# Kernel tuning notes

Hardware: AMD Instinct MI355X
Metric: run time of the kernel (lower is better)

Reference implementation:

```python
import jax, jax.numpy as jnp
import numpy as np
from jax import lax


def binarize_weight(w):
    # per-output-channel scaling alpha = mean(|w|), binary weight = sign(w)*alpha
    alpha = jnp.mean(jnp.abs(w), axis=(1, 2, 3), keepdims=True)  # [O,1,1,1]
    wb = jnp.sign(w) * alpha
    # STE: forward uses wb, gradient passes straight through to w
    return w + lax.stop_gradient(wb - w)


def pixel_unshuffle2(x):
    # NCHW, factor 2: out[:, c*4 + i*2 + j] = x[:, c, i::2, j::2]
    B, C, H, W = x.shape
    x = x.reshape(B, C, H // 2, 2, W // 2, 2)
    x = x.transpose(0, 1, 3, 5, 2, 4)
    return x.reshape(B, C * 4, H // 2, W // 2)


def setup_inputs() -> dict:
    key = jax.random.key(0)
    ks = jax.random.split(key, 5)
    x = jax.random.normal(ks[0], (16, 256, 128, 128), dtype=jnp.float32)
    conv_w = jax.random.normal(ks[1], (128, 256, 3, 3), dtype=jnp.float32) * 0.05
    move1_b = jax.random.normal(ks[2], (128,), dtype=jnp.float32) * 0.01
    prelu_w = jax.random.uniform(ks[3], (128,), dtype=jnp.float32) * 0.25
    move2_b = jax.random.normal(ks[4], (128,), dtype=jnp.float32) * 0.01
    scale = jnp.ones((1,), dtype=jnp.float32)
    return {"x": x, "conv_w": conv_w, "move1_b": move1_b,
            "prelu_w": prelu_w, "move2_b": move2_b, "scale": scale}


def reference(x, conv_w, move1_b, prelu_w, move2_b, scale):
    wb = binarize_weight(conv_w)
    out = lax.conv_general_dilated(
        x, wb, window_strides=(1, 1), padding=((1, 1), (1, 1)),
        dimension_numbers=("NCHW", "OIHW", "NCHW"))  # [B,128,H,W]
    out = out + move1_b[None, :, None, None]
    a = prelu_w[None, :, None, None]
    out = jnp.where(out > 0, out, a * out)
    out = out + move2_b[None, :, None, None]
    shortcut = x[:, : x.shape[1] // 2, :, :] * scale[0]
    out = out + shortcut
    return pixel_unshuffle2(out)  # [B,512,H/2,W/2]
```

## Files before the change

### kernel.cpp

```cpp
#include <hip/hip_runtime.h>
#include <stdint.h>

typedef unsigned short ushort_t;
typedef __bf16 bf16x8 __attribute__((ext_vector_type(8)));
typedef float f32x4 __attribute__((ext_vector_type(4)));

#define NB   16
#define CIN  256
#define COUT 128
#define HH   128
#define WW   128
#define HP   130
#define WP   130
#define KTAP 9
#define KTOT 2304

__device__ __forceinline__ ushort_t f2bf(float f) {
  union { float f; uint32_t u; } v; v.f = f;
  uint32_t u = v.u;
  uint32_t r = (u + 0x7fffu + ((u >> 16) & 1u)) >> 16;
  return (ushort_t)r;
}
__device__ __forceinline__ float bf2f(ushort_t b) {
  union { uint32_t u; float f; } v; v.u = ((uint32_t)b) << 16;
  return v.f;
}
__device__ __forceinline__ void gload_lds16(const void* g, void* l) {
  __builtin_amdgcn_global_load_lds((const __attribute__((address_space(1))) void*)g,
                                   (__attribute__((address_space(3))) void*)l, 16, 0, 0);
}

__global__ void prep_w_kernel(const float* __restrict__ w,
                              ushort_t* __restrict__ sgnW,
                              float* __restrict__ alpha) {
  int o = blockIdx.x, t = threadIdx.x;
  float s = 0.f;
  for (int e = t; e < KTOT; e += 256) {
    float v = w[o * KTOT + e];
    s += fabsf(v);
    ushort_t sg = (v > 0.f) ? 0x3F80 : (v < 0.f ? 0xBF80 : 0);
    int c = e / 9;
    int tap = e - c * 9;
    sgnW[(tap * COUT + o) * CIN + c] = sg;
  }
  __shared__ float red[4];
  for (int off = 32; off; off >>= 1) s += __shfl_down(s, off, 64);
  if ((t & 63) == 0) red[t >> 6] = s;
  __syncthreads();
  if (t == 0) alpha[o] = (red[0] + red[1] + red[2] + red[3]) / (float)KTOT;
}

__global__ void transpose_kernel(const float* __restrict__ x,
                                 ushort_t* __restrict__ xT) {
  int bid = blockIdx.x;
  int ct = bid & 3;
  int wt = (bid >> 2) & 1;
  int h  = (bid >> 3) & 127;
  int b  = bid >> 10;
  int c0 = ct * 64, w0 = wt * 64;
  __shared__ float tile[64][65];
  int t = threadIdx.x;
  int wl = t & 63, cl4 = t >> 6;
  const float* src = x + (((size_t)b * CIN + c0) * HH + h) * WW + w0;
  for (int it = 0; it < 16; ++it) {
    int cl = it * 4 + cl4;
    tile[cl][wl] = src[(size_t)cl * (HH * WW) + wl];
  }
  __syncthreads();
  int cp = t & 31, wi = t >> 5;
  for (int it = 0; it < 8; ++it) {
    int wl2 = it * 8 + wi;
    int cl = cp * 2;
    uint32_t pk = (uint32_t)f2bf(tile[cl][wl2]) |
                  ((uint32_t)f2bf(tile[cl + 1][wl2]) << 16);
    size_t idx = ((((size_t)b * HP + h + 1) * WP) + (w0 + wl2 + 1)) * CIN + c0 + cl;
    *(uint32_t*)(xT + idx) = pk;
  }
}

__global__ __launch_bounds__(256, 2) void conv_gemm(
    const ushort_t* __restrict__ xT, const ushort_t* __restrict__ sgnW,
    const float* __restrict__ alpha, const float* __restrict__ mv1,
    const float* __restrict__ pw, const float* __restrict__ mv2,
    const float* __restrict__ scale, float* __restrict__ out) {
  __shared__ __align__(16) ushort_t As[128 * 64];
  __shared__ __align__(16) ushort_t Bs[128 * 64];

  int bid = blockIdx.x;
  int wg = ((bid & 7) << 8) | (bid >> 3);
  int b = wg >> 7, h = wg & 127;

  int t = threadIdx.x, wv = t >> 6, l = t & 63;
  int wr = wv >> 1, wc = wv & 1;

  int crow = l >> 3;
  int se = (l & 7) ^ crow;

  f32x4 acc[4][4] = {};

  const ushort_t* xb = xT + ((size_t)b * HP + h) * WP * CIN;

  for (int ks = 0; ks < 36; ++ks) {
    int tap = ks >> 2, i0 = (ks & 3) << 6;
    int kh = (tap >= 6) ? 2 : (tap >= 3 ? 1 : 0);
    int kw = tap - kh * 3;
    __syncthreads();
    const ushort_t* gA = xb + (kh * WP + kw) * CIN + i0 + se * 8;
    const ushort_t* gB = sgnW + tap * (COUT * CIN) + i0 + se * 8;
#pragma unroll
    for (int q = 0; q < 4; ++q) {
      int c = wv * 4 + q;
      int m = c * 8 + crow;
      gload_lds16(gA + (size_t)m * CIN, (char*)As + c * 1024);
      gload_lds16(gB + (size_t)m * CIN, (char*)Bs + c * 1024);
    }
    __syncthreads();
#pragma unroll
    for (int kk = 0; kk < 2; ++kk) {
      bf16x8 av[4], bv[4];
      int lg = l >> 4, rA = l & 15;
#pragma unroll
      for (int mi = 0; mi < 4; ++mi) {
        int m = wr * 64 + mi * 16 + rA;
        int slot = (kk * 4 + lg) ^ (m & 7);
        av[mi] = *(const bf16x8*)((const char*)As + m * 128 + slot * 16);
      }
#pragma unroll
      for (int ni = 0; ni < 4; ++ni) {
        int o = wc * 64 + ni * 16 + rA;
        int slot = (kk * 4 + lg) ^ (o & 7);
        bv[ni] = *(const bf16x8*)((const char*)Bs + o * 128 + slot * 16);
      }
#pragma unroll
      for (int mi = 0; mi < 4; ++mi)
#pragma unroll
        for (int ni = 0; ni < 4; ++ni)
          acc[mi][ni] = __builtin_amdgcn_mfma_f32_16x16x32_bf16(av[mi], bv[ni], acc[mi][ni], 0, 0, 0);
    }
  }

  float sc0 = scale[0];
  int lg = l >> 4, rA = l & 15;
  const ushort_t* scrow = xT + (((size_t)b * HP + h + 1) * WP + 1) * CIN;
  size_t outBase = (((size_t)b * 512 + (h & 1) * 2) * 64 + (h >> 1)) * 64;
#pragma unroll
  for (int ni = 0; ni < 4; ++ni) {
    int o = wc * 64 + ni * 16 + rA;
    float al = alpha[o], b1 = mv1[o], p = pw[o], b2 = mv2[o];
#pragma unroll
    for (int mi = 0; mi < 4; ++mi) {
#pragma unroll
      for (int r = 0; r < 4; ++r) {
        int w = wr * 64 + mi * 16 + lg * 4 + r;
        float v = acc[mi][ni][r] * al + b1;
        v = v > 0.f ? v : p * v;
        v += b2;
        v += bf2f(scrow[(size_t)w * CIN + o]) * sc0;
        out[outBase + (size_t)(o * 4 + (w & 1)) * 4096 + (w >> 1)] = v;
      }
    }
  }
}

extern "C" void kernel_launch(void* const* d_in, const int* in_sizes, int n_in,
                              void* d_out, int out_size, void* d_ws, size_t ws_size,
                              hipStream_t stream) {
  const float* x      = (const float*)d_in[0];
  const float* conv_w = (const float*)d_in[1];
  const float* mv1    = (const float*)d_in[2];
  const float* pw     = (const float*)d_in[3];
  const float* mv2    = (const float*)d_in[4];
  const float* scale  = (const float*)d_in[5];
  float* out = (float*)d_out;

  const size_t XT_ELEMS = (size_t)NB * HP * WP * CIN;
  ushort_t* xT   = (ushort_t*)d_ws;
  ushort_t* sgnW = xT + XT_ELEMS;
  float*    alpha = (float*)(sgnW + (size_t)KTAP * COUT * CIN);

  prep_w_kernel<<<COUT, 256, 0, stream>>>(conv_w, sgnW, alpha);
  hipMemsetAsync(xT, 0, XT_ELEMS * sizeof(ushort_t), stream);
  transpose_kernel<<<NB * HH * 2 * 4, 256, 0, stream>>>(x, xT);
  conv_gemm<<<NB * HH, 256, 0, stream>>>(xT, sgnW, alpha, mv1, pw, mv2, scale, out);
}
```

Before: 657.0 us.

## Double-buffer conv GEMM LDS loads, zero only padding, vectorize transpose stores

The conv GEMM now double-buffers its A/B LDS tiles, so the next k-step's global-to-LDS loads are in flight while the current step's MFMAs run. It uses explicit vmcnt waits and raw barriers, and reorders the k loop to go tap-fastest within each channel block. The full-buffer memset is replaced by a kernel that zeroes only the padding border. The transpose writes 16-byte packed stores, and the weight prep is restructured so each thread handles one input channel. LDS use doubles to 64KB per block, which may cap occupancy at the requested two blocks per CU.

```diff
diff --git a/kernel.cpp b/kernel.cpp
--- a/kernel.cpp
+++ b/kernel.cpp
@@ -33,21 +33,34 @@
 __global__ void prep_w_kernel(const float* __restrict__ w,
                               ushort_t* __restrict__ sgnW,
                               float* __restrict__ alpha) {
-  int o = blockIdx.x, t = threadIdx.x;
+  int o = blockIdx.x, c = threadIdx.x;
+  const float* wo = w + (size_t)o * KTOT + c * 9;
   float s = 0.f;
-  for (int e = t; e < KTOT; e += 256) {
-    float v = w[o * KTOT + e];
+#pragma unroll
+  for (int tap = 0; tap < 9; ++tap) {
+    float v = wo[tap];
     s += fabsf(v);
     ushort_t sg = (v > 0.f) ? 0x3F80 : (v < 0.f ? 0xBF80 : 0);
-    int c = e / 9;
-    int tap = e - c * 9;
-    sgnW[(tap * COUT + o) * CIN + c] = sg;
+    sgnW[((size_t)tap * COUT + o) * CIN + c] = sg;
   }
   __shared__ float red[4];
   for (int off = 32; off; off >>= 1) s += __shfl_down(s, off, 64);
-  if ((t & 63) == 0) red[t >> 6] = s;
+  if (!(c & 63)) red[c >> 6] = s;
   __syncthreads();
-  if (t == 0) alpha[o] = (red[0] + red[1] + red[2] + red[3]) / (float)KTOT;
+  if (!c) alpha[o] = (red[0] + red[1] + red[2] + red[3]) * (1.f / (float)KTOT);
+}
+
+__global__ void pad_kernel(ushort_t* __restrict__ xT) {
+  int blk = blockIdx.x;
+  int b = blk / 130, h = blk - b * 130;
+  int t = threadIdx.x;
+  uint32_t* row = (uint32_t*)(xT + ((size_t)b * HP + h) * WP * CIN);
+  if (h == 0 || h == 129) {
+    for (int i = t; i < WP * CIN / 2; i += 256) row[i] = 0;
+  } else {
+    if (t < 128) row[t] = 0;
+    else         row[129 * (CIN / 2) + (t - 128)] = 0;
+  }
 }
 
 __global__ void transpose_kernel(const float* __restrict__ x,
@@ -60,21 +73,25 @@
   int c0 = ct * 64, w0 = wt * 64;
   __shared__ float tile[64][65];
   int t = threadIdx.x;
-  int wl = t & 63, cl4 = t >> 6;
   const float* src = x + (((size_t)b * CIN + c0) * HH + h) * WW + w0;
+#pragma unroll 4
   for (int it = 0; it < 16; ++it) {
-    int cl = it * 4 + cl4;
-    tile[cl][wl] = src[(size_t)cl * (HH * WW) + wl];
+    int cl = it * 4 + (t >> 6);
+    tile[cl][t & 63] = src[(size_t)cl * (HH * WW) + (t & 63)];
   }
   __syncthreads();
-  int cp = t & 31, wi = t >> 5;
-  for (int it = 0; it < 8; ++it) {
-    int wl2 = it * 8 + wi;
-    int cl = cp * 2;
-    uint32_t pk = (uint32_t)f2bf(tile[cl][wl2]) |
-                  ((uint32_t)f2bf(tile[cl + 1][wl2]) << 16);
-    size_t idx = ((((size_t)b * HP + h + 1) * WP) + (w0 + wl2 + 1)) * CIN + c0 + cl;
-    *(uint32_t*)(xT + idx) = pk;
+  int cb = (t & 7) * 8;
+  int wl = t >> 3;
+#pragma unroll
+  for (int wp = 0; wp < 2; ++wp) {
+    int w = wp * 32 + wl;
+    uint32_t pk[4];
+#pragma unroll
+    for (int j = 0; j < 4; ++j)
+      pk[j] = (uint32_t)f2bf(tile[cb + 2 * j][w]) |
+              ((uint32_t)f2bf(tile[cb + 2 * j + 1][w]) << 16);
+    size_t idx = ((((size_t)b * HP + h + 1) * WP) + (w0 + w + 1)) * CIN + c0 + cb;
+    *(uint4*)(xT + idx) = *(uint4*)pk;
   }
 }
 
@@ -83,8 +100,8 @@
     const float* __restrict__ alpha, const float* __restrict__ mv1,
     const float* __restrict__ pw, const float* __restrict__ mv2,
     const float* __restrict__ scale, float* __restrict__ out) {
-  __shared__ __align__(16) ushort_t As[128 * 64];
-  __shared__ __align__(16) ushort_t Bs[128 * 64];
+  __shared__ __align__(16) ushort_t As[2][128 * 64];
+  __shared__ __align__(16) ushort_t Bs[2][128 * 64];
 
   int bid = blockIdx.x;
   int wg = ((bid & 7) << 8) | (bid >> 3);
@@ -95,41 +112,54 @@
 
   int crow = l >> 3;
   int se = (l & 7) ^ crow;
+  int lg = l >> 4, rA = l & 15;
 
   f32x4 acc[4][4] = {};
 
   const ushort_t* xb = xT + ((size_t)b * HP + h) * WP * CIN;
 
+#define STAGE(ksv, buf)                                                        \
+  {                                                                            \
+    int i0q_ = (ksv) / 9, tap_ = (ksv) - 9 * i0q_;                             \
+    int kh_ = tap_ / 3, kw_ = tap_ - kh_ * 3;                                  \
+    const ushort_t* gA_ = xb + (kh_ * WP + kw_) * CIN + (i0q_ << 6) + se * 8;  \
+    const ushort_t* gB_ = sgnW + (size_t)tap_ * (COUT * CIN) + (i0q_ << 6) + se * 8; \
+    _Pragma("unroll")                                                          \
+    for (int q = 0; q < 4; ++q) {                                              \
+      int c_ = wv * 4 + q;                                                     \
+      int m_ = c_ * 8 + crow;                                                  \
+      gload_lds16(gA_ + (size_t)m_ * CIN, (char*)&As[buf][0] + c_ * 1024);     \
+      gload_lds16(gB_ + (size_t)m_ * CIN, (char*)&Bs[buf][0] + c_ * 1024);     \
+    }                                                                          \
+  }
+
+  STAGE(0, 0);
   for (int ks = 0; ks < 36; ++ks) {
-    int tap = ks >> 2, i0 = (ks & 3) << 6;
-    int kh = (tap >= 6) ? 2 : (tap >= 3 ? 1 : 0);
-    int kw = tap - kh * 3;
-    __syncthreads();
-    const ushort_t* gA = xb + (kh * WP + kw) * CIN + i0 + se * 8;
-    const ushort_t* gB = sgnW + tap * (COUT * CIN) + i0 + se * 8;
-#pragma unroll
-    for (int q = 0; q < 4; ++q) {
-      int c = wv * 4 + q;
-      int m = c * 8 + crow;
-      gload_lds16(gA + (size_t)m * CIN, (char*)As + c * 1024);
-      gload_lds16(gB + (size_t)m * CIN, (char*)Bs + c * 1024);
+    int cur = ks & 1;
+    if (ks < 35) {
+      STAGE(ks + 1, cur ^ 1);
+      asm volatile("s_waitcnt vmcnt(8)" ::: "memory");
+    } else {
+      asm volatile("s_waitcnt vmcnt(0)" ::: "memory");
     }
-    __syncthreads();
+    __builtin_amdgcn_s_barrier();
+    asm volatile("" ::: "memory");
+    const char* Ab = (const char*)&As[0][0] + cur * (128 * 64 * 2);
+    const char* Bb = (const char*)&Bs[0][0] + cur * (128 * 64 * 2);
 #pragma unroll
     for (int kk = 0; kk < 2; ++kk) {
       bf16x8 av[4], bv[4];
-      int lg = l >> 4, rA = l & 15;
 #pragma unroll
       for (int mi = 0; mi < 4; ++mi) {
         int m = wr * 64 + mi * 16 + rA;
         int slot = (kk * 4 + lg) ^ (m & 7);
-        av[mi] = *(const bf16x8*)((const char*)As + m * 128 + slot * 16);
+        av[mi] = *(const bf16x8*)(Ab + m * 128 + slot * 16);
       }
 #pragma unroll
       for (int ni = 0; ni < 4; ++ni) {
         int o = wc * 64 + ni * 16 + rA;
         int slot = (kk * 4 + lg) ^ (o & 7);
-        bv[ni] = *(const bf16x8*)((const char*)Bs + o * 128 + slot * 16);
+        bv[ni] = *(const bf16x8*)(Bb + o * 128 + slot * 16);
       }
 #pragma unroll
       for (int mi = 0; mi < 4; ++mi)
@@ -137,10 +167,11 @@
         for (int ni = 0; ni < 4; ++ni)
           acc[mi][ni] = __builtin_amdgcn_mfma_f32_16x16x32_bf16(av[mi], bv[ni], acc[mi][ni], 0, 0, 0);
     }
+    __builtin_amdgcn_s_barrier();
+    asm volatile("" ::: "memory");
   }
 
   float sc0 = scale[0];
-  int lg = l >> 4, rA = l & 15;
   const ushort_t* scrow = xT + (((size_t)b * HP + h + 1) * WP + 1) * CIN;
   size_t outBase = (((size_t)b * 512 + (h & 1) * 2) * 64 + (h >> 1)) * 64;
 #pragma unroll
@@ -179,7 +210,7 @@
   float*    alpha = (float*)(sgnW + (size_t)KTAP * COUT * CIN);
 
   prep_w_kernel<<<COUT, 256, 0, stream>>>(conv_w, sgnW, alpha);
-  hipMemsetAsync(xT, 0, XT_ELEMS * sizeof(ushort_t), stream);
+  pad_kernel<<<NB * HP, 256, 0, stream>>>(xT);
   transpose_kernel<<<NB * HH * 2 * 4, 256, 0, stream>>>(x, xT);
   conv_gemm<<<NB * HH, 256, 0, stream>>>(xT, sgnW, alpha, mv1, pw, mv2, scale, out);
 }
```

Result: slower. 673.2 us (+2.5%).
